# Kernel tuning notes

Measured on AMD Instinct MI355X. Metric: run time of the kernel, lower is better.

Reference implementation:

```python
import jax, jax.numpy as jnp
import numpy as np

V = 5023      # CoMA mesh vertices
K = 8         # avg neighbors per vertex
E = V * K     # edges
B = 64        # batch
C_IN = 3      # xyz
C_HID = 64    # conv width (layer_info)
M = 9         # kernel_size: number of weight matrices
LATENT = 128


def fsc_conv(x, src, dst, aw, u, c, W, b):
    """Feature-steered graph conv (translation invariant: v = -u).
    x: [B,V,C]; edge e: (i=src[e], j=dst[e]) with adjacency weight aw[e].
    y_i = b + sum_j a_ij * sum_m softmax_m(u_m.(x_i-x_j)+c_m) * (x_j @ W_m)
    """
    Bx, Vx, C = x.shape
    D = W.shape[2]
    xi = x[:, src]                                  # [B,E,C]
    xj = x[:, dst]                                  # [B,E,C]
    logits = jnp.einsum('bec,cm->bem', xi - xj, u) + c   # [B,E,M]
    att = jax.nn.softmax(logits, axis=-1) * aw[None, :, None]
    y = jnp.zeros((Bx, Vx, D), x.dtype)
    for m in range(W.shape[0]):                     # small fixed loop over M
        agg = jnp.zeros((Bx, Vx, C), x.dtype).at[:, src].add(att[:, :, m:m + 1] * xj)
        y = y + agg @ W[m]
    return y + b


def setup_inputs() -> dict:
    key = jax.random.key(0)
    ks = jax.random.split(key, 16)
    x = jax.random.normal(ks[0], (B, V, C_IN), jnp.float32)
    # mesh-like adjacency: each vertex i has K random neighbors, weight 1/K
    src = jnp.repeat(jnp.arange(V, dtype=jnp.int32), K)
    dst = jax.random.randint(ks[1], (E,), 0, V, dtype=jnp.int32)
    aw = jnp.full((E,), 1.0 / K, jnp.float32)
    g = lambda k, shp, fan: jax.random.normal(k, shp, jnp.float32) * np.float32(np.sqrt(2.0 / fan))
    # encoder conv params
    u_e = g(ks[2], (C_IN, M), C_IN + M)
    c_e = jnp.zeros((M,), jnp.float32)
    W_e = g(ks[3], (M, C_IN, C_HID), C_IN + C_HID)
    b_e = jnp.zeros((C_HID,), jnp.float32)
    # encoder latent dense: [V*C_HID, LATENT]
    W_enc = g(ks[4], (V * C_HID, LATENT), V * C_HID)
    b_enc = jnp.zeros((LATENT,), jnp.float32)
    # decoder latent dense: [LATENT, C_HID*V]
    W_dec = g(ks[5], (LATENT, C_HID * V), LATENT)
    b_dec = jnp.zeros((C_HID * V,), jnp.float32)
    # decoder conv params
    u_d = g(ks[6], (C_HID, M), C_HID + M)
    c_d = jnp.zeros((M,), jnp.float32)
    W_d = g(ks[7], (M, C_HID, C_IN), C_HID + C_IN)
    b_d = jnp.zeros((C_IN,), jnp.float32)
    return {'x': x, 'aw': aw, 'u_e': u_e, 'c_e': c_e, 'W_e': W_e, 'b_e': b_e,
            'W_enc': W_enc, 'b_enc': b_enc, 'W_dec': W_dec, 'b_dec': b_dec,
            'u_d': u_d, 'c_d': c_d, 'W_d': W_d, 'b_d': b_d,
            'src': src, 'dst': dst}


def reference(x, aw, u_e, c_e, W_e, b_e, W_enc, b_enc, W_dec, b_dec,
              u_d, c_d, W_d, b_d, src, dst):
    # Encoder: feature-steered conv -> relu -> flatten -> dense to latent
    h = jax.nn.relu(fsc_conv(x, src, dst, aw, u_e, c_e, W_e, b_e))   # [B,V,C_HID]
    z = h.reshape(h.shape[0], -1) @ W_enc + b_enc                    # [B,LATENT]
    # Decoder: dense -> reshape [B,V,C_HID] -> feature-steered conv -> relu
    d = (z @ W_dec + b_dec).reshape(z.shape[0], V, -1)               # [B,V,C_HID]
    out = jax.nn.relu(fsc_conv(d, src, dst, aw, u_d, c_d, W_d, b_d)) # [B,V,3]
    return out
```

## Files before the change

### kernel.cpp

```cpp
#include <hip/hip_runtime.h>

#define VN 5023
#define KN 8
#define BN 64
#define CIN 3
#define CH 64
#define MN 9
#define LAT 128
#define KTOT (VN*CH)
#define NBV (BN*VN)
#define KC 256
#define NCHUNK 1256
#define RED_G 8
#define RED_J 157
#define NXCD 8

__global__ __launch_bounds__(256, 4) void k_conv1(
    const float* __restrict__ x, const float* __restrict__ aw,
    const int* __restrict__ dst,
    const float* __restrict__ u_e, const float* __restrict__ c_e,
    const float* __restrict__ W_e, const float* __restrict__ b_e,
    float* __restrict__ h)
{
  int t = blockIdx.x*256 + threadIdx.x;
  if (t >= NBV) return;
  int b = t / VN, v = t - b*VN;
  const float* xb = x + (size_t)b*VN*CIN;
  int e0 = v*KN;
  int4 j01 = *(const int4*)(dst + e0);
  int4 j23 = *(const int4*)(dst + e0 + 4);
  int jj[8] = {j01.x,j01.y,j01.z,j01.w, j23.x,j23.y,j23.z,j23.w};
  float4 a01 = *(const float4*)(aw + e0);
  float4 a23 = *(const float4*)(aw + e0 + 4);
  float awv[8] = {a01.x,a01.y,a01.z,a01.w, a23.x,a23.y,a23.z,a23.w};
  float xj0[8], xj1[8], xj2[8];
#pragma unroll
  for (int k=0;k<KN;k++){
    const float* xr = xb + (size_t)jj[k]*3;
    xj0[k]=xr[0]; xj1[k]=xr[1]; xj2[k]=xr[2];
  }
  __builtin_amdgcn_sched_barrier(0);
  float xi0 = xb[v*3+0], xi1 = xb[v*3+1], xi2 = xb[v*3+2];
  float Ti[MN];
#pragma unroll
  for (int m=0;m<MN;m++)
    Ti[m] = xi0*u_e[m] + xi1*u_e[MN+m] + xi2*u_e[2*MN+m] + c_e[m];
  float agg[27];
#pragma unroll
  for (int i=0;i<27;i++) agg[i]=0.f;
#pragma unroll
  for (int k=0;k<KN;k++){
    float lg[MN];
#pragma unroll
    for (int m=0;m<MN;m++)
      lg[m] = Ti[m] - (xj0[k]*u_e[m]+xj1[k]*u_e[MN+m]+xj2[k]*u_e[2*MN+m]);
    float mx = lg[0];
#pragma unroll
    for (int m=1;m<MN;m++) mx = fmaxf(mx, lg[m]);
    float ex[MN], s=0.f;
#pragma unroll
    for (int m=0;m<MN;m++){ ex[m] = __expf(lg[m]-mx); s += ex[m]; }
    float r = awv[k] / s;
#pragma unroll
    for (int m=0;m<MN;m++){
      float a = ex[m]*r;
      agg[m*3+0] += a*xj0[k]; agg[m*3+1] += a*xj1[k]; agg[m*3+2] += a*xj2[k];
    }
  }
  float* hr = h + (size_t)t*CH;
  for (int cc=0; cc<4; cc++){
    float y[16];
#pragma unroll
    for (int c=0;c<16;c++) y[c] = b_e[cc*16+c];
#pragma unroll
    for (int mc=0; mc<27; mc++){
      float a = agg[mc];
#pragma unroll
      for (int c=0;c<16;c++) y[c] += a * W_e[mc*CH + cc*16 + c];
    }
#pragma unroll
    for (int c=0;c<16;c+=4){
      float4 o = make_float4(fmaxf(y[c],0.f),fmaxf(y[c+1],0.f),
                             fmaxf(y[c+2],0.f),fmaxf(y[c+3],0.f));
      *(float4*)(hr + cc*16 + c) = o;
    }
  }
}

__global__ __launch_bounds__(256, 4) void k_enc(
    const float* __restrict__ h, const float* __restrict__ We,
    float* __restrict__ partial)
{
  __shared__ float wlds[2][32*128];
  __shared__ float hlds[2][32][68];
  int t = threadIdx.x;
  int blk = blockIdx.x;
  int lq = t & 15;
  int bq = t >> 4;
  float acc[8][4];
#pragma unroll
  for (int i=0;i<8;i++)
#pragma unroll
    for (int j=0;j<4;j++) acc[i][j]=0.f;
  int kbase0 = blk*KC;
  int ldb = t & 63;
  int seg = t >> 6;
  int nt0 = (blk == NCHUNK-1) ? 6 : 8;

  float4 wreg0, wreg1, wreg2, wreg3, hreg0, hreg1;
  {
    const float* wsrc = We + (size_t)kbase0*LAT;
    wreg0 = *(const float4*)(wsrc + 0*1024 + t*4);
    wreg1 = *(const float4*)(wsrc + 1*1024 + t*4);
    wreg2 = *(const float4*)(wsrc + 2*1024 + t*4);
    wreg3 = *(const float4*)(wsrc + 3*1024 + t*4);
    const float* hsrc = h + (size_t)ldb*KTOT + kbase0 + seg*8;
    hreg0 = *(const float4*)(hsrc);
    hreg1 = *(const float4*)(hsrc + 4);
    *(float4*)(&wlds[0][0*1024 + t*4]) = wreg0;
    *(float4*)(&wlds[0][1*1024 + t*4]) = wreg1;
    *(float4*)(&wlds[0][2*1024 + t*4]) = wreg2;
    *(float4*)(&wlds[0][3*1024 + t*4]) = wreg3;
    hlds[0][seg*8+0][ldb]=hreg0.x; hlds[0][seg*8+1][ldb]=hreg0.y;
    hlds[0][seg*8+2][ldb]=hreg0.z; hlds[0][seg*8+3][ldb]=hreg0.w;
    hlds[0][seg*8+4][ldb]=hreg1.x; hlds[0][seg*8+5][ldb]=hreg1.y;
    hlds[0][seg*8+6][ldb]=hreg1.z; hlds[0][seg*8+7][ldb]=hreg1.w;
  }
  __syncthreads();

  int cur = 0;
  for (int t0=0; t0<nt0; t0++){
    bool pf = (t0+1 < nt0);
    if (pf){
      int kbase = kbase0 + (t0+1)*32;
      const float* wsrc = We + (size_t)kbase*LAT;
      wreg0 = *(const float4*)(wsrc + 0*1024 + t*4);
      wreg1 = *(const float4*)(wsrc + 1*1024 + t*4);
      wreg2 = *(const float4*)(wsrc + 2*1024 + t*4);
      wreg3 = *(const float4*)(wsrc + 3*1024 + t*4);
      const float* hsrc = h + (size_t)ldb*KTOT + kbase + seg*8;
      hreg0 = *(const float4*)(hsrc);
      hreg1 = *(const float4*)(hsrc + 4);
    }
    __builtin_amdgcn_sched_barrier(0);
#pragma unroll 4
    for (int kk=0; kk<32; kk++){
      float4 w0 = *(const float4*)(&wlds[cur][kk*128 + lq*4]);
      float4 w1 = *(const float4*)(&wlds[cur][kk*128 + 64 + lq*4]);
      float4 z  = *(const float4*)(&hlds[cur][kk][bq*4]);
      float wv[8] = {w0.x,w0.y,w0.z,w0.w,w1.x,w1.y,w1.z,w1.w};
      float zv[4] = {z.x,z.y,z.z,z.w};
#pragma unroll
      for (int li=0;li<8;li++)
#pragma unroll
        for (int bi=0;bi<4;bi++) acc[li][bi] += wv[li]*zv[bi];
    }
    if (pf){
      int nb = cur^1;
      *(float4*)(&wlds[nb][0*1024 + t*4]) = wreg0;
      *(float4*)(&wlds[nb][1*1024 + t*4]) = wreg1;
      *(float4*)(&wlds[nb][2*1024 + t*4]) = wreg2;
      *(float4*)(&wlds[nb][3*1024 + t*4]) = wreg3;
      hlds[nb][seg*8+0][ldb]=hreg0.x; hlds[nb][seg*8+1][ldb]=hreg0.y;
      hlds[nb][seg*8+2][ldb]=hreg0.z; hlds[nb][seg*8+3][ldb]=hreg0.w;
      hlds[nb][seg*8+4][ldb]=hreg1.x; hlds[nb][seg*8+5][ldb]=hreg1.y;
      hlds[nb][seg*8+6][ldb]=hreg1.z; hlds[nb][seg*8+7][ldb]=hreg1.w;
    }
    __syncthreads();
    cur ^= 1;
  }
  float* pp = partial + (size_t)blk*(BN*LAT);
#pragma unroll
  for (int bi=0;bi<4;bi++){
    int b = bq*4+bi;
    float4 o0 = make_float4(acc[0][bi],acc[1][bi],acc[2][bi],acc[3][bi]);
    float4 o1 = make_float4(acc[4][bi],acc[5][bi],acc[6][bi],acc[7][bi]);
    *(float4*)(pp + b*LAT + lq*4)      = o0;
    *(float4*)(pp + b*LAT + 64 + lq*4) = o1;
  }
}

__global__ __launch_bounds__(256) void k_red1(
    const float* __restrict__ partial, float* __restrict__ partial2)
{
  int idx = blockIdx.x*256 + threadIdx.x;
  int g = blockIdx.y;
  float s = 0.f;
  for (int j=0;j<RED_J;j++)
    s += partial[(size_t)(g + RED_G*j)*(BN*LAT) + idx];
  partial2[(size_t)g*(BN*LAT) + idx] = s;
}

__global__ __launch_bounds__(256) void k_red2(
    const float* __restrict__ partial2, const float* __restrict__ b_enc,
    float* __restrict__ zT)
{
  int idx = blockIdx.x*256 + threadIdx.x;
  float s = 0.f;
#pragma unroll
  for (int g=0; g<RED_G; g++) s += partial2[(size_t)g*(BN*LAT) + idx];
  int b = idx >> 7, l = idx & 127;
  zT[l*BN + b] = s + b_enc[l];
}

__global__ __launch_bounds__(256, 4) void k_dectg(
    const float* __restrict__ zT, const float* __restrict__ Wd,
    const float* __restrict__ b_dec, const float* __restrict__ u_d,
    const float* __restrict__ W_d, float* __restrict__ TG)
{
  __shared__ float4 dt4[4][512];
  int t = threadIdx.x;
  int lane = t & 63;
  int wv = __builtin_amdgcn_readfirstlane(t >> 6);
  int blk = blockIdx.x;
  int vc = blk*256 + lane*4;
  int vs = vc < (KTOT-4) ? vc : (KTOT-4);
  const float* wp = Wd + vs;
  const float* zrow = zT + wv*16;
  float acc[4][16];
#pragma unroll
  for (int i=0;i<4;i++)
#pragma unroll
    for (int j=0;j<16;j++) acc[i][j]=0.f;

  float4 wA[4], wB[4];
#pragma unroll
  for (int u=0;u<4;u++) wA[u] = *(const float4*)(wp + (size_t)u*KTOT);

  for (int l0=0; l0<LAT; l0+=8){
#pragma unroll
    for (int u=0;u<4;u++) wB[u] = *(const float4*)(wp + (size_t)(l0+4+u)*KTOT);
    __builtin_amdgcn_sched_barrier(0);
#pragma unroll
    for (int u=0;u<4;u++){
      int l = l0+u;
      float zv[16];
#pragma unroll
      for (int j=0;j<16;j++) zv[j] = zrow[l*BN + j];
      float wvv[4] = {wA[u].x,wA[u].y,wA[u].z,wA[u].w};
#pragma unroll
      for (int i=0;i<4;i++)
#pragma unroll
        for (int j=0;j<16;j++) acc[i][j] += wvv[i]*zv[j];
    }
    if (l0+8 < LAT){
#pragma unroll
      for (int u=0;u<4;u++) wA[u] = *(const float4*)(wp + (size_t)(l0+8+u)*KTOT);
    }
    __builtin_amdgcn_sched_barrier(0);
#pragma unroll
    for (int u=0;u<4;u++){
      int l = l0+4+u;
      float zv[16];
#pragma unroll
      for (int j=0;j<16;j++) zv[j] = zrow[l*BN + j];
      float wvv[4] = {wB[u].x,wB[u].y,wB[u].z,wB[u].w};
#pragma unroll
      for (int i=0;i<4;i++)
#pragma unroll
        for (int j=0;j<16;j++) acc[i][j] += wvv[i]*zv[j];
    }
  }
  float4 bd = *(const float4*)(b_dec + vs);
  float bdv[4] = {bd.x, bd.y, bd.z, bd.w};
  int chb = lane & 15;
  int vl4 = lane >> 4;

#pragma unroll
  for (int hh=0; hh<2; hh++){
#pragma unroll
    for (int jj=0; jj<8; jj++){
      int j = hh*8 + jj;
      dt4[wv][vl4*128 + jj*16 + (chb^jj)] =
        make_float4(acc[0][j]+bdv[0], acc[1][j]+bdv[1],
                    acc[2][j]+bdv[2], acc[3][j]+bdv[3]);
    }
    __syncthreads();
    if (lane < 32){
      int vl = lane >> 3, bl = lane & 7;
      int vg = blk*4 + vl;
      if (vg < VN){
        float Tg[36];
#pragma unroll
        for (int q=0;q<36;q++) Tg[q]=0.f;
#pragma unroll 1
        for (int cb=0; cb<16; cb++){
          float4 dq = dt4[wv][vl*128 + bl*16 + (cb^bl)];
          float dv4[4] = {dq.x,dq.y,dq.z,dq.w};
#pragma unroll
          for (int ii=0; ii<4; ii++){
            int c = cb*4 + ii;
            float dv = dv4[ii];
            const float* ur = u_d + c*MN;
#pragma unroll
            for (int m=0;m<MN;m++) Tg[m] += dv*ur[m];
#pragma unroll
            for (int m=0;m<MN;m++){
              const float* wr = W_d + (m*CH + c)*3;
              Tg[9+m*3+0] += dv*wr[0];
              Tg[9+m*3+1] += dv*wr[1];
              Tg[9+m*3+2] += dv*wr[2];
            }
          }
        }
        int bg = wv*16 + hh*8 + bl;
        float* tg = TG + (size_t)((size_t)bg*VN + vg)*36;
#pragma unroll
        for (int q=0;q<9;q++)
          *(float4*)(tg + q*4) = make_float4(Tg[q*4+0],Tg[q*4+1],
                                             Tg[q*4+2],Tg[q*4+3]);
      }
    }
    __syncthreads();
  }
}

__global__ __launch_bounds__(256, 4) void k_att(
    const float* __restrict__ TG, const float* __restrict__ aw,
    const int* __restrict__ dst, const float* __restrict__ c_d,
    const float* __restrict__ b_d, float* __restrict__ out)
{
  int wg = blockIdx.x;
  int wgid = (wg & 7)*157 + (wg >> 3);
  int t = wgid*256 + threadIdx.x;
  if (t >= NBV) return;
  int b = t / VN, v = t - b*VN;
  const float* TGb = TG + (size_t)b*VN*36;
  int e0 = v*KN;
  int4 j01 = *(const int4*)(dst + e0);
  int4 j23 = *(const int4*)(dst + e0 + 4);
  int jj[8] = {j01.x,j01.y,j01.z,j01.w, j23.x,j23.y,j23.z,j23.w};
  float4 a01 = *(const float4*)(aw + e0);
  float4 a23 = *(const float4*)(aw + e0 + 4);
  float awv[8] = {a01.x,a01.y,a01.z,a01.w, a23.x,a23.y,a23.z,a23.w};
  float Ti[MN];
#pragma unroll
  for (int m=0;m<MN;m++) Ti[m] = TGb[(size_t)v*36+m] + c_d[m];
  float y0=0.f, y1=0.f, y2=0.f;
  float4 q[9];
  {
    const float* Rp = TGb + (size_t)jj[0]*36;
#pragma unroll
    for (int i=0;i<9;i++) q[i] = *(const float4*)(Rp + i*4);
  }
#pragma unroll
  for (int k=0;k<KN;k++){
    float4 p[9];
    if (k+1 < KN){
      const float* Rp = TGb + (size_t)jj[k+1]*36;
#pragma unroll
      for (int i=0;i<9;i++) p[i] = *(const float4*)(Rp + i*4);
    }
    float rr[36] = {q[0].x,q[0].y,q[0].z,q[0].w, q[1].x,q[1].y,q[1].z,q[1].w,
                    q[2].x,q[2].y,q[2].z,q[2].w, q[3].x,q[3].y,q[3].z,q[3].w,
                    q[4].x,q[4].y,q[4].z,q[4].w, q[5].x,q[5].y,q[5].z,q[5].w,
                    q[6].x,q[6].y,q[6].z,q[6].w, q[7].x,q[7].y,q[7].z,q[7].w,
                    q[8].x,q[8].y,q[8].z,q[8].w};
    float lg[MN];
#pragma unroll
    for (int m=0;m<MN;m++) lg[m] = Ti[m] - rr[m];
    float mx = lg[0];
#pragma unroll
    for (int m=1;m<MN;m++) mx = fmaxf(mx, lg[m]);
    float ex[MN], s=0.f;
#pragma unroll
    for (int m=0;m<MN;m++){ ex[m] = __expf(lg[m]-mx); s += ex[m]; }
    float sc = awv[k] / s;
#pragma unroll
    for (int m=0;m<MN;m++){
      float a = ex[m]*sc;
      y0 += a*rr[9+m*3+0]; y1 += a*rr[9+m*3+1]; y2 += a*rr[9+m*3+2];
    }
    if (k+1 < KN){
#pragma unroll
      for (int i=0;i<9;i++) q[i] = p[i];
    }
  }
  float* o = out + (size_t)t*3;
  o[0]=fmaxf(y0+b_d[0],0.f); o[1]=fmaxf(y1+b_d[1],0.f); o[2]=fmaxf(y2+b_d[2],0.f);
}

extern "C" void kernel_launch(void* const* d_in, const int* in_sizes, int n_in,
                              void* d_out, int out_size, void* d_ws, size_t ws_size,
                              hipStream_t stream) {
  const float* x     = (const float*)d_in[0];
  const float* aw    = (const float*)d_in[1];
  const float* u_e   = (const float*)d_in[2];
  const float* c_e   = (const float*)d_in[3];
  const float* W_e   = (const float*)d_in[4];
  const float* b_e   = (const float*)d_in[5];
  const float* W_enc = (const float*)d_in[6];
  const float* b_enc = (const float*)d_in[7];
  const float* W_dec = (const float*)d_in[8];
  const float* b_dec = (const float*)d_in[9];
  const float* u_d   = (const float*)d_in[10];
  const float* c_d   = (const float*)d_in[11];
  const float* W_d   = (const float*)d_in[12];
  const float* b_d   = (const float*)d_in[13];
  const int*   dst   = (const int*)d_in[15];
  float* out = (float*)d_out;

  char* ws = (char*)d_ws;
  float* hbuf = (float*)ws;
  float* zT   = (float*)ws;
  float* partial2 = (float*)(ws + (64<<10));
  size_t off1 = (size_t)NBV*CH*sizeof(float);
  float* partial = (float*)(ws + off1);
  float* TGbuf   = (float*)(ws + off1);

  int grid_bv = (NBV + 255)/256;

  k_conv1<<<grid_bv,256,0,stream>>>(x, aw, dst, u_e, c_e, W_e, b_e, hbuf);
  k_enc<<<NCHUNK,256,0,stream>>>(hbuf, W_enc, partial);
  dim3 gr1(32, RED_G);
  k_red1<<<gr1,256,0,stream>>>(partial, partial2);
  k_red2<<<32,256,0,stream>>>(partial2, b_enc, zT);
  int grid_dec = (KTOT + 255)/256;
  k_dectg<<<grid_dec,256,0,stream>>>(zT, W_dec, b_dec, u_d, W_d, TGbuf);
  k_att<<<grid_bv,256,0,stream>>>(TGbuf, aw, dst, c_d, b_d, out);
}
```

Measured before the change: 310.1 us.

## Enlarge k_enc per-thread tile to 8x8 with 128-thread blocks; raise dectg occupancy

The encoder GEMM kernel now runs 128 threads per block, and each thread accumulates an 8x8 output tile instead of 8x4. Global-to-LDS staging is widened to match, so each thread loads eight W float4 and four h float4 per stage. The aim is more FMA work per LDS read and fewer threads, at the cost of higher register pressure and less latency hiding. Separately, k_dectg's launch-bounds hint goes from 4 to 8 blocks per CU, which asks the compiler to cap registers for higher occupancy and may cause spills.

```diff
diff --git a/kernel.cpp b/kernel.cpp
--- a/kernel.cpp
+++ b/kernel.cpp
@@ -87,7 +87,7 @@
   }
 }
 
-__global__ __launch_bounds__(256, 4) void k_enc(
+__global__ __launch_bounds__(128, 4) void k_enc(
     const float* __restrict__ h, const float* __restrict__ We,
     float* __restrict__ partial)
 {
@@ -97,34 +97,31 @@
   int blk = blockIdx.x;
   int lq = t & 15;
   int bq = t >> 4;
-  float acc[8][4];
+  float acc[8][8];
 #pragma unroll
   for (int i=0;i<8;i++)
 #pragma unroll
-    for (int j=0;j<4;j++) acc[i][j]=0.f;
+    for (int j=0;j<8;j++) acc[i][j]=0.f;
   int kbase0 = blk*KC;
   int ldb = t & 63;
   int seg = t >> 6;
   int nt0 = (blk == NCHUNK-1) ? 6 : 8;
 
-  float4 wreg0, wreg1, wreg2, wreg3, hreg0, hreg1;
+  float4 wreg[8], hreg[4];
   {
     const float* wsrc = We + (size_t)kbase0*LAT;
-    wreg0 = *(const float4*)(wsrc + 0*1024 + t*4);
-    wreg1 = *(const float4*)(wsrc + 1*1024 + t*4);
-    wreg2 = *(const float4*)(wsrc + 2*1024 + t*4);
-    wreg3 = *(const float4*)(wsrc + 3*1024 + t*4);
-    const float* hsrc = h + (size_t)ldb*KTOT + kbase0 + seg*8;
-    hreg0 = *(const float4*)(hsrc);
-    hreg1 = *(const float4*)(hsrc + 4);
-    *(float4*)(&wlds[0][0*1024 + t*4]) = wreg0;
-    *(float4*)(&wlds[0][1*1024 + t*4]) = wreg1;
-    *(float4*)(&wlds[0][2*1024 + t*4]) = wreg2;
-    *(float4*)(&wlds[0][3*1024 + t*4]) = wreg3;
-    hlds[0][seg*8+0][ldb]=hreg0.x; hlds[0][seg*8+1][ldb]=hreg0.y;
-    hlds[0][seg*8+2][ldb]=hreg0.z; hlds[0][seg*8+3][ldb]=hreg0.w;
-    hlds[0][seg*8+4][ldb]=hreg1.x; hlds[0][seg*8+5][ldb]=hreg1.y;
-    hlds[0][seg*8+6][ldb]=hreg1.z; hlds[0][seg*8+7][ldb]=hreg1.w;
+#pragma unroll
+    for (int q=0;q<8;q++) wreg[q] = *(const float4*)(wsrc + (q*128+t)*4);
+    const float* hsrc = h + (size_t)ldb*KTOT + kbase0 + seg*16;
+#pragma unroll
+    for (int q=0;q<4;q++) hreg[q] = *(const float4*)(hsrc + q*4);
+#pragma unroll
+    for (int q=0;q<8;q++) *(float4*)(&wlds[0][(q*128+t)*4]) = wreg[q];
+#pragma unroll
+    for (int q=0;q<4;q++){
+      hlds[0][seg*16+q*4+0][ldb]=hreg[q].x; hlds[0][seg*16+q*4+1][ldb]=hreg[q].y;
+      hlds[0][seg*16+q*4+2][ldb]=hreg[q].z; hlds[0][seg*16+q*4+3][ldb]=hreg[q].w;
+    }
   }
   __syncthreads();
 
@@ -134,45 +131,43 @@
     if (pf){
       int kbase = kbase0 + (t0+1)*32;
       const float* wsrc = We + (size_t)kbase*LAT;
-      wreg0 = *(const float4*)(wsrc + 0*1024 + t*4);
-      wreg1 = *(const float4*)(wsrc + 1*1024 + t*4);
-      wreg2 = *(const float4*)(wsrc + 2*1024 + t*4);
-      wreg3 = *(const float4*)(wsrc + 3*1024 + t*4);
-      const float* hsrc = h + (size_t)ldb*KTOT + kbase + seg*8;
-      hreg0 = *(const float4*)(hsrc);
-      hreg1 = *(const float4*)(hsrc + 4);
+#pragma unroll
+      for (int q=0;q<8;q++) wreg[q] = *(const float4*)(wsrc + (q*128+t)*4);
+      const float* hsrc = h + (size_t)ldb*KTOT + kbase + seg*16;
+#pragma unroll
+      for (int q=0;q<4;q++) hreg[q] = *(const float4*)(hsrc + q*4);
     }
     __builtin_amdgcn_sched_barrier(0);
 #pragma unroll 4
     for (int kk=0; kk<32; kk++){
       float4 w0 = *(const float4*)(&wlds[cur][kk*128 + lq*4]);
       float4 w1 = *(const float4*)(&wlds[cur][kk*128 + 64 + lq*4]);
-      float4 z  = *(const float4*)(&hlds[cur][kk][bq*4]);
+      float4 z0 = *(const float4*)(&hlds[cur][kk][bq*8]);
+      float4 z1 = *(const float4*)(&hlds[cur][kk][bq*8+4]);
       float wv[8] = {w0.x,w0.y,w0.z,w0.w,w1.x,w1.y,w1.z,w1.w};
-      float zv[4] = {z.x,z.y,z.z,z.w};
+      float zv[8] = {z0.x,z0.y,z0.z,z0.w,z1.x,z1.y,z1.z,z1.w};
 #pragma unroll
       for (int li=0;li<8;li++)
 #pragma unroll
-        for (int bi=0;bi<4;bi++) acc[li][bi] += wv[li]*zv[bi];
+        for (int bi=0;bi<8;bi++) acc[li][bi] += wv[li]*zv[bi];
     }
     if (pf){
       int nb = cur^1;
-      *(float4*)(&wlds[nb][0*1024 + t*4]) = wreg0;
-      *(float4*)(&wlds[nb][1*1024 + t*4]) = wreg1;
-      *(float4*)(&wlds[nb][2*1024 + t*4]) = wreg2;
-      *(float4*)(&wlds[nb][3*1024 + t*4]) = wreg3;
-      hlds[nb][seg*8+0][ldb]=hreg0.x; hlds[nb][seg*8+1][ldb]=hreg0.y;
-      hlds[nb][seg*8+2][ldb]=hreg0.z; hlds[nb][seg*8+3][ldb]=hreg0.w;
-      hlds[nb][seg*8+4][ldb]=hreg1.x; hlds[nb][seg*8+5][ldb]=hreg1.y;
-      hlds[nb][seg*8+6][ldb]=hreg1.z; hlds[nb][seg*8+7][ldb]=hreg1.w;
+#pragma unroll
+      for (int q=0;q<8;q++) *(float4*)(&wlds[nb][(q*128+t)*4]) = wreg[q];
+#pragma unroll
+      for (int q=0;q<4;q++){
+        hlds[nb][seg*16+q*4+0][ldb]=hreg[q].x; hlds[nb][seg*16+q*4+1][ldb]=hreg[q].y;
+        hlds[nb][seg*16+q*4+2][ldb]=hreg[q].z; hlds[nb][seg*16+q*4+3][ldb]=hreg[q].w;
+      }
     }
     __syncthreads();
     cur ^= 1;
   }
   float* pp = partial + (size_t)blk*(BN*LAT);
 #pragma unroll
-  for (int bi=0;bi<4;bi++){
-    int b = bq*4+bi;
+  for (int bi=0;bi<8;bi++){
+    int b = bq*8+bi;
     float4 o0 = make_float4(acc[0][bi],acc[1][bi],acc[2][bi],acc[3][bi]);
     float4 o1 = make_float4(acc[4][bi],acc[5][bi],acc[6][bi],acc[7][bi]);
     *(float4*)(pp + b*LAT + lq*4)      = o0;
@@ -203,7 +198,7 @@
   zT[l*BN + b] = s + b_enc[l];
 }
 
-__global__ __launch_bounds__(256, 4) void k_dectg(
+__global__ __launch_bounds__(256, 8) void k_dectg(
     const float* __restrict__ zT, const float* __restrict__ Wd,
     const float* __restrict__ b_dec, const float* __restrict__ u_d,
     const float* __restrict__ W_d, float* __restrict__ TG)
@@ -411,7 +406,7 @@
   int grid_bv = (NBV + 255)/256;
 
   k_conv1<<<grid_bv,256,0,stream>>>(x, aw, dst, u_e, c_e, W_e, b_e, hbuf);
-  k_enc<<<NCHUNK,256,0,stream>>>(hbuf, W_enc, partial);
+  k_enc<<<NCHUNK,128,0,stream>>>(hbuf, W_enc, partial);
   dim3 gr1(32, RED_G);
   k_red1<<<gr1,256,0,stream>>>(partial, partial2);
   k_red2<<<32,256,0,stream>>>(partial2, b_enc, zT);
```

Result: slower. 353.9 us (+14.1%).
